# Optimization experiments

Hardware: AMD Instinct MI355X
Metric: run time of the kernel (lower is better)

Reference implementation:

```python
import math
import jax, jax.numpy as jnp
import numpy as np

B, N, D, H = 2, 2048, 1024, 16
HD = D // H  # 64
TWO_PI = 2.0 * math.pi
ROPE_BASE = 10000.0


def setup_inputs() -> dict:
    key = jax.random.key(0)
    ks = jax.random.split(key, 8)
    s = 0.02
    x = jax.random.normal(ks[0], (B, N, D), dtype=jnp.float32)
    Wq = jax.random.normal(ks[1], (D, D), dtype=jnp.float32) * s
    Wk = jax.random.normal(ks[2], (D, D), dtype=jnp.float32) * s
    Wv = jax.random.normal(ks[3], (D, D), dtype=jnp.float32) * s
    Wo = jax.random.normal(ks[4], (D, D), dtype=jnp.float32) * s
    cw = jax.random.normal(ks[5], (D,), dtype=jnp.float32) * s  # complexity_proj weight
    cb = jnp.zeros((), dtype=jnp.float32)                        # complexity_proj bias
    alpha = jnp.asarray(0.1, dtype=jnp.float32)
    T_base = jnp.asarray(10.0, dtype=jnp.float32)
    root_ids = jax.random.randint(ks[6], (B, N), 0, 1000)
    mask = jnp.tril(jnp.ones((N, N), dtype=jnp.int32))  # causal
    return {"x": x, "Wq": Wq, "Wk": Wk, "Wv": Wv, "Wo": Wo,
            "alpha": alpha, "T_base": T_base, "cw": cw, "cb": cb,
            "root_ids": root_ids, "mask": mask, "t_step": 3}


def _rope_cos_sin(seq_len, head_dim, dtype):
    inv_freq = 1.0 / (ROPE_BASE ** (jnp.arange(0, head_dim, 2, dtype=jnp.float32) / head_dim))
    pos = jnp.arange(seq_len, dtype=jnp.float32)
    freqs = pos[:, None] * inv_freq[None, :]          # (N, HD/2)
    emb = jnp.concatenate([freqs, freqs], axis=-1)    # (N, HD)
    return jnp.cos(emb).astype(dtype), jnp.sin(emb).astype(dtype)


def _rotate_half(t):
    half = t.shape[-1] // 2
    return jnp.concatenate([-t[..., half:], t[..., :half]], axis=-1)


def reference(x, Wq, Wk, Wv, Wo, alpha, T_base, cw, cb, root_ids, mask, t_step):
    b, n, d = x.shape
    # QKV projection -> (B, H, N, HD)
    def proj(W):
        return jnp.einsum('bnd,ed->bne', x, W).reshape(b, n, H, HD).transpose(0, 2, 1, 3)
    q, k, v = proj(Wq), proj(Wk), proj(Wv)
    # RoPE
    cos, sin = _rope_cos_sin(n, HD, x.dtype)          # (N, HD)
    q = q * cos + _rotate_half(q) * sin
    k = k * cos + _rotate_half(k) * sin
    # Per-sample temperature via complexity + cardiac oscillation
    complexity = jax.nn.sigmoid(jnp.einsum('bd,d->b', x.mean(axis=1), cw) + cb)  # (B,)
    T_eff = (jnp.abs(T_base) + 1.0) * (0.5 + complexity)                          # (B,)
    psi = 1.0 + alpha * jnp.sin(TWO_PI * t_step / T_eff)                          # (B,)
    scale = (math.sqrt(HD) * psi)[:, None, None, None]                            # (B,1,1,1)
    # Attention with full NxN scores (eager path, as in source)
    scores = jnp.einsum('bhqd,bhkd->bhqk', q, k) / scale
    scores = jnp.where(mask[None, None, :, :] == 0, -jnp.inf, scores)
    attn = jax.nn.softmax(scores, axis=-1)
    out = jnp.einsum('bhqk,bhkd->bhqd', attn, v)       # (B,H,N,HD)
    out = out.transpose(0, 2, 1, 3).reshape(b, n, d)
    return jnp.einsum('bnd,ed->bne', out, Wo)
```

## Files before the change

### kernel.cpp

```cpp
#include <hip/hip_runtime.h>


typedef short short8 __attribute__((ext_vector_type(8)));
typedef float floatx4 __attribute__((ext_vector_type(4)));
typedef float f32x16 __attribute__((ext_vector_type(16)));
typedef unsigned int uint4v __attribute__((ext_vector_type(4)));
typedef unsigned int u32x4v __attribute__((ext_vector_type(4)));
typedef unsigned short us4 __attribute__((ext_vector_type(4)));
typedef unsigned short u16;

#define DEV __device__ __forceinline__

#define GLOAD16(g, l)                                                      \
  __builtin_amdgcn_global_load_lds(                                        \
      (const __attribute__((address_space(1))) void*)(g),                  \
      (__attribute__((address_space(3))) void*)(l), 16, 0, 0)

static const int Bb = 2;

static const size_t OFF_XB = 0;
static const size_t OFF_WQ = 8388608;
static const size_t OFF_WK = OFF_WQ + 2097152;
static const size_t OFF_WV = OFF_WK + 2097152;
static const size_t OFF_WO = OFF_WV + 2097152;
static const size_t OFF_Q  = OFF_WO + 2097152;
static const size_t OFF_K  = OFF_Q + 8388608;
static const size_t OFF_V  = OFF_K + 8388608;
static const size_t OFF_AO = OFF_V + 8388608;
static const size_t OFF_SC = OFF_AO + 8388608;

DEV u16 f2bf(float f) {
  unsigned int u = __builtin_bit_cast(unsigned int, f);
  u += 0x7fffu + ((u >> 16) & 1u);
  return (u16)(u >> 16);
}

DEV unsigned pkbf(float lo, float hi) {
  unsigned r;
  asm("v_cvt_pk_bf16_f32 %0, %1, %2" : "=v"(r) : "v"(lo), "v"(hi));
  return r;
}

__global__ __launch_bounds__(256) void cvt_all_kernel(
    const float* __restrict__ x, const float* __restrict__ wq,
    const float* __restrict__ wk, const float* __restrict__ wv,
    const float* __restrict__ wo, const float* __restrict__ cw,
    u16* __restrict__ xb, u16* __restrict__ wqb, u16* __restrict__ wkb,
    u16* __restrict__ wvb, u16* __restrict__ wob, float* __restrict__ part) {
  const int blk = blockIdx.x;
  if (blk < 4096) {
    int i = blk * 256 + threadIdx.x;
    float4 f = ((const float4*)x)[i];
    us4 o;
    o[0] = f2bf(f.x); o[1] = f2bf(f.y); o[2] = f2bf(f.z); o[3] = f2bf(f.w);
    ((us4*)xb)[i] = o;
    float4 c = ((const float4*)cw)[i & 255];
    float acc = f.x * c.x + f.y * c.y + f.z * c.z + f.w * c.w;
    __shared__ float red[256];
    red[threadIdx.x] = acc;
    __syncthreads();
    for (int s = 128; s > 0; s >>= 1) {
      if (threadIdx.x < s) red[threadIdx.x] += red[threadIdx.x + s];
      __syncthreads();
    }
    if (threadIdx.x == 0) atomicAdd(&part[blk >> 11], red[0]);
  } else {
    int r = blk - 4096;
    int wi = r >> 10;
    int i = (r & 1023) * 256 + threadIdx.x;
    const float* src = (wi == 0) ? wq : (wi == 1) ? wk : (wi == 2) ? wv : wo;
    u16* dst = (wi == 0) ? wqb : (wi == 1) ? wkb : (wi == 2) ? wvb : wob;
    float4 f = ((const float4*)src)[i];
    us4 o;
    o[0] = f2bf(f.x); o[1] = f2bf(f.y); o[2] = f2bf(f.z); o[3] = f2bf(f.w);
    ((us4*)dst)[i] = o;
  }
}

__global__ void scale_finalize_kernel(const float* __restrict__ part,
                                      const float* __restrict__ cb,
                                      const float* __restrict__ alpha,
                                      const float* __restrict__ tb,
                                      const int* __restrict__ tstep,
                                      float* __restrict__ out) {
  int b = threadIdx.x;
  if (b >= Bb) return;
  float sm = part[b] * (1.0f / 2048.0f) + cb[0];
  float cx = 1.0f / (1.0f + expf(-sm));
  float Te = (fabsf(tb[0]) + 1.0f) * (0.5f + cx);
  float psi = 1.0f + alpha[0] * sinf(6.283185307179586f * (float)tstep[0] / Te);
  out[b] = 1.0f / (8.0f * psi);
}

__global__ void rope_table_kernel(float2* __restrict__ rt) {
  int i = blockIdx.x * 256 + threadIdx.x;
  int pos = i >> 5, hd2 = i & 31;
  float ang = (float)pos * exp2f(-(float)hd2 * 0.41524101186092030f);
  float sv, cv;
  sincosf(ang, &sv, &cv);
  rt[i] = make_float2(cv, sv);
}

__global__ __launch_bounds__(256) void gemm_qkv_kernel(
    const u16* __restrict__ xb, const u16* __restrict__ wq, const u16* __restrict__ wk,
    const u16* __restrict__ wv, const float2* __restrict__ rt,
    u16* __restrict__ q, u16* __restrict__ k, u16* __restrict__ v) {
  const int tm = blockIdx.x, tn = blockIdx.y, which = blockIdx.z;
  const u16* W = (which == 0) ? wq : (which == 1) ? wk : wv;
  u16* dst = (which == 0) ? q : (which == 1) ? k : v;

  __shared__ __align__(16) u16 As[128 * 32];
  __shared__ __align__(16) u16 Bs[128 * 32];

  const int t = threadIdx.x, lane = t & 63, w = t >> 6;
  const int wm = w >> 1, wn = w & 1, lg = lane >> 4, lr = lane & 15;

  floatx4 acc[4][4];
#pragma unroll
  for (int i = 0; i < 4; i++)
#pragma unroll
    for (int j = 0; j < 4; j++) acc[i][j] = (floatx4){0.f, 0.f, 0.f, 0.f};

  const int rowA = tm * 128, rowB = tn * 128;
  const u16* gA = xb + (size_t)(rowA + w * 32 + (lane >> 2)) * 1024 + (lane & 3) * 8;
  const u16* gB = W + (size_t)(rowB + w * 32 + (lane >> 2)) * 1024 + (lane & 3) * 8;
  u16* lA = As + w * 1024;
  u16* lB = Bs + w * 1024;

  for (int kt = 0; kt < 32; ++kt) {
    GLOAD16(gA, lA);
    GLOAD16(gA + 16 * 1024, lA + 512);
    GLOAD16(gB, lB);
    GLOAD16(gB + 16 * 1024, lB + 512);
    __syncthreads();
    short8 af[4], bw[4];
#pragma unroll
    for (int i = 0; i < 4; i++)
      af[i] = *(const short8*)(As + (wm * 64 + i * 16 + lr) * 32 + lg * 8);
#pragma unroll
    for (int j = 0; j < 4; j++)
      bw[j] = *(const short8*)(Bs + (wn * 64 + j * 16 + lr) * 32 + lg * 8);
#pragma unroll
    for (int i = 0; i < 4; i++)
#pragma unroll
      for (int j = 0; j < 4; j++)
        acc[i][j] = __builtin_amdgcn_mfma_f32_16x16x32_bf16(af[i], bw[j], acc[i][j], 0, 0, 0);
    __syncthreads();
    gA += 32; gB += 32;
  }

  const int rowbase = tm * 128 + wm * 64, colbase = tn * 128 + wn * 64;
  if (which <= 1) {
#pragma unroll
    for (int i = 0; i < 4; i++)
#pragma unroll
      for (int ii = 0; ii < 4; ii++) {
        int gm = rowbase + i * 16 + lg * 4 + ii;
        int pos = gm & 2047, bb = gm >> 11;
#pragma unroll
        for (int jp = 0; jp < 2; jp++) {
          int hd2 = jp * 16 + lr;
          float2 cs = rt[pos * 32 + hd2];
          float a0 = acc[i][jp][ii], a1 = acc[i][jp + 2][ii];
          int e0 = colbase + jp * 16 + lr;
          int hh = e0 >> 6;
          size_t base = (((size_t)bb * 16 + hh) * 2048 + pos) * 64;
          dst[base + hd2]      = f2bf(a0 * cs.x - a1 * cs.y);
          dst[base + hd2 + 32] = f2bf(a1 * cs.x + a0 * cs.y);
        }
      }
  } else {
#pragma unroll
    for (int i = 0; i < 4; i++)
#pragma unroll
      for (int ii = 0; ii < 4; ii++) {
        int gm = rowbase + i * 16 + lg * 4 + ii;
        int pos = gm & 2047, bb = gm >> 11;
#pragma unroll
        for (int j = 0; j < 4; j++) {
          int ge = colbase + j * 16 + lr;
          int hh = ge >> 6, hd = ge & 63;
          dst[(((size_t)bb * 16 + hh) * 2048 + pos) * 64 + hd] = f2bf(acc[i][j][ii]);
        }
      }
  }
}

__global__ __launch_bounds__(256) void vtrans_kernel(const u16* __restrict__ v,
                                                     u16* __restrict__ vt) {
  const int bh = blockIdx.x, nt = blockIdx.y;
  __shared__ __align__(16) u16 T[64 * 64];
  const int t = threadIdx.x;
  const size_t vi = (size_t)bh * 131072 + (size_t)nt * 4096;
#pragma unroll
  for (int s = 0; s < 2; s++) {
    int g = s * 256 + t, n = g >> 3, dc = g & 7;
    *(uint4v*)(T + n * 64 + ((dc ^ (n & 7)) * 8)) =
        *(const uint4v*)(v + vi + (size_t)n * 64 + dc * 8);
  }
  __syncthreads();
  const size_t vo = (size_t)bh * 131072 + (size_t)nt * 64;
#pragma unroll
  for (int s = 0; s < 2; s++) {
    int g = s * 256 + t, nc = g & 7, d = g >> 3;
    short8 o;
#pragma unroll
    for (int jj = 0; jj < 8; jj++) {
      int n = nc * 8 + jj;
      o[jj] = (short)T[n * 64 + (((d >> 3) ^ (n & 7)) * 8) + (d & 7)];
    }
    *(short8*)(vt + vo + (size_t)d * 2048 + nc * 8) = o;
  }
}

__global__ __launch_bounds__(256) void attn_kernel(
    const u16* __restrict__ q, const u16* __restrict__ k, const u16* __restrict__ vt,
    u16* __restrict__ ao, const float* __restrict__ scale_ws) {
  const int bid = blockIdx.x;
  const int swz = (bid & 7) * 64 + (bid >> 3);
  const int bh = swz >> 4, p = swz & 15;
  const int b = bh >> 4, h = bh & 15;
  const int w = threadIdx.x >> 6, lane = threadIdx.x & 63;
  const int l31 = lane & 31, hi = lane >> 5;
  const int tsel = (w == 0) ? p : (w == 1) ? 31 - p : (w == 2) ? 32 + p : 63 - p;
  const int q0 = tsel * 32;
  const int KT = tsel >> 1;
  const float isc2 = scale_ws[b] * 1.4426950408889634f;
  const size_t koff = (size_t)bh * 131072;
  const float NINF = -__builtin_inff();

  short8 bq[4];
#pragma unroll
  for (int k4 = 0; k4 < 4; k4++)
    bq[k4] = *(const short8*)(q + koff + (size_t)(q0 + l31) * 64 + k4 * 16 + hi * 8);

  f32x16 o0, o1;
#pragma unroll
  for (int r = 0; r < 16; r++) { o0[r] = 0.f; o1[r] = 0.f; }
  float m2 = NINF, ell = 0.f;

  for (int kt = 0; kt <= KT; ++kt) {
    const int cbase = kt << 6;
    const bool haveMt1 = (cbase + 32 <= q0 + 31);

    short8 ka0[4], ka1[4];
#pragma unroll
    for (int k4 = 0; k4 < 4; k4++)
      ka0[k4] = *(const short8*)(k + koff + (size_t)(cbase + l31) * 64 + k4 * 16 + hi * 8);
    if (haveMt1) {
#pragma unroll
      for (int k4 = 0; k4 < 4; k4++)
        ka1[k4] = *(const short8*)(k + koff + (size_t)(cbase + 32 + l31) * 64 + k4 * 16 + hi * 8);
    }
    const int nct = haveMt1 ? 4 : 2;
    short8 va0[4], va1[4];
#pragma unroll
    for (int ct = 0; ct < 4; ct++) {
      if (ct < nct) {
        va0[ct] = *(const short8*)(vt + koff + (size_t)l31 * 2048 + cbase + ct * 16 + hi * 8);
        va1[ct] = *(const short8*)(vt + koff + (size_t)(32 + l31) * 2048 + cbase + ct * 16 + hi * 8);
      }
    }

    f32x16 s0, s1;
#pragma unroll
    for (int r = 0; r < 16; r++) { s0[r] = 0.f; s1[r] = 0.f; }
#pragma unroll
    for (int k4 = 0; k4 < 4; k4++)
      s0 = __builtin_amdgcn_mfma_f32_32x32x16_bf16(ka0[k4], bq[k4], s0, 0, 0, 0);
    if (haveMt1) {
#pragma unroll
      for (int k4 = 0; k4 < 4; k4++)
        s1 = __builtin_amdgcn_mfma_f32_32x32x16_bf16(ka1[k4], bq[k4], s1, 0, 0, 0);
    }

#pragma unroll
    for (int r = 0; r < 16; r++) { s0[r] *= isc2; s1[r] *= isc2; }
    if (kt == KT) {
      const int thr = q0 + l31 - cbase;
#pragma unroll
      for (int r = 0; r < 16; r++) {
        const int crow = (r & 3) + 8 * (r >> 2) + 4 * hi;
        if (crow > thr) s0[r] = NINF;
        if (crow + 32 > thr) s1[r] = NINF;
      }
    }

    float mx = s0[0];
#pragma unroll
    for (int r = 1; r < 16; r++) mx = fmaxf(mx, s0[r]);
#pragma unroll
    for (int r = 0; r < 16; r++) mx = fmaxf(mx, s1[r]);
    mx = fmaxf(mx, __shfl_xor(mx, 32, 64));
    const float mn = fmaxf(m2, mx);
    const float rsc = exp2f(m2 - mn);
    m2 = mn;
    f32x16 p0, p1;
    float ps = 0.f;
#pragma unroll
    for (int r = 0; r < 16; r++) { p0[r] = exp2f(s0[r] - mn); ps += p0[r]; }
#pragma unroll
    for (int r = 0; r < 16; r++) { p1[r] = exp2f(s1[r] - mn); ps += p1[r]; }
    ps += __shfl_xor(ps, 32, 64);
    ell = ell * rsc + ps;
#pragma unroll
    for (int r = 0; r < 16; r++) { o0[r] *= rsc; o1[r] *= rsc; }

#pragma unroll
    for (int ct = 0; ct < 4; ct++) {
      if (ct < nct) {
        const f32x16& pp = (ct < 2) ? p0 : p1;
        const int rA = (ct & 1) * 8;
        unsigned pkA0 = pkbf(pp[rA + 0], pp[rA + 1]);
        unsigned pkA1 = pkbf(pp[rA + 2], pp[rA + 3]);
        unsigned pkB0 = pkbf(pp[rA + 4], pp[rA + 5]);
        unsigned pkB1 = pkbf(pp[rA + 6], pp[rA + 7]);
        unsigned u0 = (unsigned)__shfl_xor((int)(hi ? pkA0 : pkB0), 32, 64);
        unsigned u1 = (unsigned)__shfl_xor((int)(hi ? pkA1 : pkB1), 32, 64);
        u32x4v pu;
        pu[0] = hi ? u0 : pkA0;
        pu[1] = hi ? u1 : pkA1;
        pu[2] = hi ? pkB0 : u0;
        pu[3] = hi ? pkB1 : u1;
        short8 pf = __builtin_bit_cast(short8, pu);
        o0 = __builtin_amdgcn_mfma_f32_32x32x16_bf16(va0[ct], pf, o0, 0, 0, 0);
        o1 = __builtin_amdgcn_mfma_f32_32x32x16_bf16(va1[ct], pf, o1, 0, 0, 0);
      }
    }
  }

  const float invl = 1.0f / ell;
  u16* orow = ao + ((size_t)(b * 2048 + q0 + l31)) * 1024 + h * 64;
#pragma unroll
  for (int qd = 0; qd < 4; qd++) {
    us4 st0, st1;
#pragma unroll
    for (int j = 0; j < 4; j++) {
      st0[j] = f2bf(o0[qd * 4 + j] * invl);
      st1[j] = f2bf(o1[qd * 4 + j] * invl);
    }
    *(us4*)(orow + qd * 8 + hi * 4) = st0;
    *(us4*)(orow + 32 + qd * 8 + hi * 4) = st1;
  }
}

__global__ __launch_bounds__(256) void gemm_out_kernel(const u16* __restrict__ ab,
                                                       const u16* __restrict__ wo,
                                                       float* __restrict__ out) {
  const int tm = blockIdx.x, tn = blockIdx.y;
  __shared__ __align__(16) u16 As[128 * 32];
  __shared__ __align__(16) u16 Bs[128 * 32];

  const int t = threadIdx.x, lane = t & 63, w = t >> 6;
  const int wm = w >> 1, wn = w & 1, lg = lane >> 4, lr = lane & 15;

  floatx4 acc[4][4];
#pragma unroll
  for (int i = 0; i < 4; i++)
#pragma unroll
    for (int j = 0; j < 4; j++) acc[i][j] = (floatx4){0.f, 0.f, 0.f, 0.f};

  const int rowA = tm * 128, rowB = tn * 128;
  const u16* gA = ab + (size_t)(rowA + w * 32 + (lane >> 2)) * 1024 + (lane & 3) * 8;
  const u16* gB = wo + (size_t)(rowB + w * 32 + (lane >> 2)) * 1024 + (lane & 3) * 8;
  u16* lA = As + w * 1024;
  u16* lB = Bs + w * 1024;

  for (int kt = 0; kt < 32; ++kt) {
    GLOAD16(gA, lA);
    GLOAD16(gA + 16 * 1024, lA + 512);
    GLOAD16(gB, lB);
    GLOAD16(gB + 16 * 1024, lB + 512);
    __syncthreads();
    short8 af[4], bw[4];
#pragma unroll
    for (int i = 0; i < 4; i++)
      af[i] = *(const short8*)(As + (wm * 64 + i * 16 + lr) * 32 + lg * 8);
#pragma unroll
    for (int j = 0; j < 4; j++)
      bw[j] = *(const short8*)(Bs + (wn * 64 + j * 16 + lr) * 32 + lg * 8);
#pragma unroll
    for (int i = 0; i < 4; i++)
#pragma unroll
      for (int j = 0; j < 4; j++)
        acc[i][j] = __builtin_amdgcn_mfma_f32_16x16x32_bf16(af[i], bw[j], acc[i][j], 0, 0, 0);
    __syncthreads();
    gA += 32; gB += 32;
  }

  const int rowbase = tm * 128 + wm * 64, colbase = tn * 128 + wn * 64;
#pragma unroll
  for (int i = 0; i < 4; i++)
#pragma unroll
    for (int ii = 0; ii < 4; ii++) {
      int gm = rowbase + i * 16 + lg * 4 + ii;
#pragma unroll
      for (int j = 0; j < 4; j++) {
        int ge = colbase + j * 16 + lr;
        out[(size_t)gm * 1024 + ge] = acc[i][j][ii];
      }
    }
}

extern "C" void kernel_launch(void* const* d_in, const int* in_sizes, int n_in,
                              void* d_out, int out_size, void* d_ws, size_t ws_size,
                              hipStream_t stream) {
  const float* x     = (const float*)d_in[0];
  const float* Wq    = (const float*)d_in[1];
  const float* Wk    = (const float*)d_in[2];
  const float* Wv    = (const float*)d_in[3];
  const float* Wo    = (const float*)d_in[4];
  const float* alpha = (const float*)d_in[5];
  const float* Tb    = (const float*)d_in[6];
  const float* cw    = (const float*)d_in[7];
  const float* cb    = (const float*)d_in[8];
  const int*   tstep = (const int*)d_in[11];

  char* ws = (char*)d_ws;
  u16* xb  = (u16*)(ws + OFF_XB);
  u16* wqb = (u16*)(ws + OFF_WQ);
  u16* wkb = (u16*)(ws + OFF_WK);
  u16* wvb = (u16*)(ws + OFF_WV);
  u16* wob = (u16*)(ws + OFF_WO);
  u16* qb  = (u16*)(ws + OFF_Q);
  u16* kb  = (u16*)(ws + OFF_K);
  u16* vb  = (u16*)(ws + OFF_V);
  u16* aob = (u16*)(ws + OFF_AO);
  u16* vtb = (u16*)(ws + OFF_XB);
  float2* rt = (float2*)(ws + OFF_AO);
  float* sc = (float*)(ws + OFF_SC);

  hipMemsetAsync(sc + 2, 0, 2 * sizeof(float), stream);

  cvt_all_kernel<<<8192, 256, 0, stream>>>(x, Wq, Wk, Wv, Wo, cw,
                                           xb, wqb, wkb, wvb, wob, sc + 2);
  scale_finalize_kernel<<<1, 64, 0, stream>>>(sc + 2, cb, alpha, Tb, tstep, sc);
  rope_table_kernel<<<256, 256, 0, stream>>>(rt);

  gemm_qkv_kernel<<<dim3(32, 8, 3), 256, 0, stream>>>(xb, wqb, wkb, wvb, rt, qb, kb, vb);

  vtrans_kernel<<<dim3(32, 32), 256, 0, stream>>>(vb, vtb);

  attn_kernel<<<dim3(512), 256, 0, stream>>>(qb, kb, vtb, aob, sc);

  gemm_out_kernel<<<dim3(32, 8), 256, 0, stream>>>(aob, wob, (float*)d_out);
}
```

Before: 307.0 us.

## Split attention KV loop across two wave groups and merge partial softmax states

The attention kernel now launches 512 threads per block. Each query tile is handled by two waves that take alternating key tiles, and the two partial (m, l, O) softmax states are merged through LDS before the output is written. This doubles the parallelism on the causal key loop and is meant to shorten the per-block critical path, at the cost of extra LDS use and a block-wide sync. Separately, both GEMM kernels drop the global_load_lds direct-to-LDS loads in favour of plain register-staged 16-byte loads into shared memory.

```diff
diff --git a/kernel.cpp b/kernel.cpp
--- a/kernel.cpp
+++ b/kernel.cpp
@@ -10,11 +10,6 @@
 typedef unsigned short u16;
 
 #define DEV __device__ __forceinline__
-
-#define GLOAD16(g, l)                                                      \
-  __builtin_amdgcn_global_load_lds(                                        \
-      (const __attribute__((address_space(1))) void*)(g),                  \
-      (__attribute__((address_space(3))) void*)(l), 16, 0, 0)
 
 static const int Bb = 2;
 
@@ -122,16 +117,16 @@
     for (int j = 0; j < 4; j++) acc[i][j] = (floatx4){0.f, 0.f, 0.f, 0.f};
 
   const int rowA = tm * 128, rowB = tn * 128;
-  const u16* gA = xb + (size_t)(rowA + w * 32 + (lane >> 2)) * 1024 + (lane & 3) * 8;
-  const u16* gB = W + (size_t)(rowB + w * 32 + (lane >> 2)) * 1024 + (lane & 3) * 8;
-  u16* lA = As + w * 1024;
-  u16* lB = Bs + w * 1024;
-
   for (int kt = 0; kt < 32; ++kt) {
-    GLOAD16(gA, lA);
-    GLOAD16(gA + 16 * 1024, lA + 512);
-    GLOAD16(gB, lB);
-    GLOAD16(gB + 16 * 1024, lB + 512);
+#pragma unroll
+    for (int s = 0; s < 2; s++) {
+      int c = t + s * 256;
+      int r = c >> 2, kc = c & 3;
+      *(uint4v*)(As + r * 32 + kc * 8) =
+          *(const uint4v*)(xb + (size_t)(rowA + r) * 1024 + kt * 32 + kc * 8);
+      *(uint4v*)(Bs + r * 32 + kc * 8) =
+          *(const uint4v*)(W + (size_t)(rowB + r) * 1024 + kt * 32 + kc * 8);
+    }
     __syncthreads();
     short8 af[4], bw[4];
 #pragma unroll
@@ -146,7 +141,6 @@
       for (int j = 0; j < 4; j++)
         acc[i][j] = __builtin_amdgcn_mfma_f32_16x16x32_bf16(af[i], bw[j], acc[i][j], 0, 0, 0);
     __syncthreads();
-    gA += 32; gB += 32;
   }
 
   const int rowbase = tm * 128 + wm * 64, colbase = tn * 128 + wn * 64;
@@ -213,7 +207,7 @@
   }
 }
 
-__global__ __launch_bounds__(256) void attn_kernel(
+__global__ __launch_bounds__(512, 4) void attn_kernel(
     const u16* __restrict__ q, const u16* __restrict__ k, const u16* __restrict__ vt,
     u16* __restrict__ ao, const float* __restrict__ scale_ws) {
   const int bid = blockIdx.x;
@@ -222,13 +216,17 @@
   const int b = bh >> 4, h = bh & 15;
   const int w = threadIdx.x >> 6, lane = threadIdx.x & 63;
   const int l31 = lane & 31, hi = lane >> 5;
-  const int tsel = (w == 0) ? p : (w == 1) ? 31 - p : (w == 2) ? 32 + p : 63 - p;
+  const int w4 = w & 3, sp = w >> 2;
+  const int tsel = (w4 == 0) ? p : (w4 == 1) ? 31 - p : (w4 == 2) ? 32 + p : 63 - p;
   const int q0 = tsel * 32;
   const int KT = tsel >> 1;
   const float isc2 = scale_ws[b] * 1.4426950408889634f;
   const size_t koff = (size_t)bh * 131072;
   const float NINF = -__builtin_inff();
 
+  __shared__ float Olds[4][64][33];
+  __shared__ float Mlds[4][2][32];
+
   short8 bq[4];
 #pragma unroll
   for (int k4 = 0; k4 < 4; k4++)
@@ -239,7 +237,7 @@
   for (int r = 0; r < 16; r++) { o0[r] = 0.f; o1[r] = 0.f; }
   float m2 = NINF, ell = 0.f;
 
-  for (int kt = 0; kt <= KT; ++kt) {
+  for (int kt = sp; kt <= KT; kt += 2) {
     const int cbase = kt << 6;
     const bool haveMt1 = (cbase + 32 <= q0 + 31);
 
@@ -329,18 +327,33 @@
     }
   }
 
-  const float invl = 1.0f / ell;
-  u16* orow = ao + ((size_t)(b * 2048 + q0 + l31)) * 1024 + h * 64;
-#pragma unroll
-  for (int qd = 0; qd < 4; qd++) {
-    us4 st0, st1;
-#pragma unroll
-    for (int j = 0; j < 4; j++) {
-      st0[j] = f2bf(o0[qd * 4 + j] * invl);
-      st1[j] = f2bf(o1[qd * 4 + j] * invl);
-    }
-    *(us4*)(orow + qd * 8 + hi * 4) = st0;
-    *(us4*)(orow + 32 + qd * 8 + hi * 4) = st1;
+  if (w >= 4) {
+#pragma unroll
+    for (int r = 0; r < 16; r++) {
+      Olds[w4][2 * r + hi][l31]      = o0[r];
+      Olds[w4][32 + 2 * r + hi][l31] = o1[r];
+    }
+    if (hi == 0) { Mlds[w4][0][l31] = m2; Mlds[w4][1][l31] = ell; }
+  }
+  __syncthreads();
+  if (w < 4) {
+    const float m_hi = Mlds[w4][0][l31], l_hi = Mlds[w4][1][l31];
+    const float mN = fmaxf(m2, m_hi);
+    const float w0 = exp2f(m2 - mN), w1 = exp2f(m_hi - mN);
+    const float invl = 1.0f / (w0 * ell + w1 * l_hi);
+    u16* orow = ao + ((size_t)(b * 2048 + q0 + l31)) * 1024 + h * 64;
+#pragma unroll
+    for (int qd = 0; qd < 4; qd++) {
+      us4 st0, st1;
+#pragma unroll
+      for (int j = 0; j < 4; j++) {
+        int r = qd * 4 + j;
+        st0[j] = f2bf((w0 * o0[r] + w1 * Olds[w4][2 * r + hi][l31]) * invl);
+        st1[j] = f2bf((w0 * o1[r] + w1 * Olds[w4][32 + 2 * r + hi][l31]) * invl);
+      }
+      *(us4*)(orow + qd * 8 + hi * 4) = st0;
+      *(us4*)(orow + 32 + qd * 8 + hi * 4) = st1;
+    }
   }
 }
 
@@ -361,16 +374,16 @@
     for (int j = 0; j < 4; j++) acc[i][j] = (floatx4){0.f, 0.f, 0.f, 0.f};
 
   const int rowA = tm * 128, rowB = tn * 128;
-  const u16* gA = ab + (size_t)(rowA + w * 32 + (lane >> 2)) * 1024 + (lane & 3) * 8;
-  const u16* gB = wo + (size_t)(rowB + w * 32 + (lane >> 2)) * 1024 + (lane & 3) * 8;
-  u16* lA = As + w * 1024;
-  u16* lB = Bs + w * 1024;
-
   for (int kt = 0; kt < 32; ++kt) {
-    GLOAD16(gA, lA);
-    GLOAD16(gA + 16 * 1024, lA + 512);
-    GLOAD16(gB, lB);
-    GLOAD16(gB + 16 * 1024, lB + 512);
+#pragma unroll
+    for (int s = 0; s < 2; s++) {
+      int c = t + s * 256;
+      int r = c >> 2, kc = c & 3;
+      *(uint4v*)(As + r * 32 + kc * 8) =
+          *(const uint4v*)(ab + (size_t)(rowA + r) * 1024 + kt * 32 + kc * 8);
+      *(uint4v*)(Bs + r * 32 + kc * 8) =
+          *(const uint4v*)(wo + (size_t)(rowB + r) * 1024 + kt * 32 + kc * 8);
+    }
     __syncthreads();
     short8 af[4], bw[4];
 #pragma unroll
@@ -385,7 +398,6 @@
       for (int j = 0; j < 4; j++)
         acc[i][j] = __builtin_amdgcn_mfma_f32_16x16x32_bf16(af[i], bw[j], acc[i][j], 0, 0, 0);
     __syncthreads();
-    gA += 32; gB += 32;
   }
 
   const int rowbase = tm * 128 + wm * 64, colbase = tn * 128 + wn * 64;
@@ -441,7 +453,7 @@
 
   vtrans_kernel<<<dim3(32, 32), 256, 0, stream>>>(vb, vtb);
 
-  attn_kernel<<<dim3(512), 256, 0, stream>>>(qb, kb, vtb, aob, sc);
+  attn_kernel<<<dim3(512), 512, 0, stream>>>(qb, kb, vtb, aob, sc);
 
   gemm_out_kernel<<<dim3(32, 8), 256, 0, stream>>>(aob, wob, (float*)d_out);
 }
```

Measured after the change: 348.2 us. 1.13x slower.
